# Kernel tuning notes

Measured on AMD Instinct MI355X. Metric: run time of the kernel, lower is better.

Reference implementation:

```python
import jax, jax.numpy as jnp
import numpy as np

NUM_LAYERS = 3
NODE_DIM = 32
TIME_DIM = 32
N_HEAD = 4
N_NODES = 1_000_000
BATCH = 256
MODEL_DIM = NODE_DIM + TIME_DIM  # 64
HEAD_DIM = MODEL_DIM // N_HEAD   # 16


def setup_inputs() -> dict:
    key = jax.random.key(0)
    ks = jax.random.split(key, 20)
    L, D, F = NUM_LAYERS, MODEL_DIM, NODE_DIM
    s = 0.1
    return {
        "src_idx": jax.random.randint(ks[0], (BATCH,), 0, N_NODES),
        "target_idx": jax.random.randint(ks[1], (BATCH,), 0, N_NODES),
        "cut_time": jax.random.uniform(ks[2], (BATCH,), dtype=jnp.float32) * 10000.0,
        "num_neighbors": 20,
        # learned params
        "emb": jax.random.uniform(ks[3], (N_NODES, F), minval=-1.0, maxval=1.0, dtype=jnp.float32),
        "time_freq": (1.0 / 10.0 ** jnp.linspace(0.0, 9.0, TIME_DIM)).astype(jnp.float32),
        "time_phase": jnp.zeros((TIME_DIM,), jnp.float32),
        "Wq": jax.random.normal(ks[4], (L, D, D), jnp.float32) * s,
        "Wk": jax.random.normal(ks[5], (L, D, D), jnp.float32) * s,
        "Wv": jax.random.normal(ks[6], (L, D, D), jnp.float32) * s,
        "Wo": jax.random.normal(ks[7], (L, D, D), jnp.float32) * s,
        "mw1": jax.random.normal(ks[8], (L, D + F, F), jnp.float32) * s,
        "mb1": jnp.zeros((L, F), jnp.float32),
        "mw2": jax.random.normal(ks[9], (L, F, F), jnp.float32) * s,
        "mb2": jnp.zeros((L, F), jnp.float32),
        "aff_w1": jax.random.normal(ks[10], (2 * F, F), jnp.float32) * s,
        "aff_b1": jnp.zeros((F,), jnp.float32),
        "aff_w2": jax.random.normal(ks[11], (F, 1), jnp.float32) * s,
        "aff_b2": jnp.zeros((1,), jnp.float32),
    }


def _time_encode(ts, freq, phase):
    # ts: [...]; output [..., TIME_DIM] harmonic encoding (TGAT TimeEncode)
    return jnp.cos(ts[..., None] * freq + phase)


def _sample_neighbors(nodes, times, num_neighbors):
    # Deterministic stand-in for ngh_finder.get_temporal_neighbor (CPU sampler).
    j = jnp.arange(num_neighbors)
    ngh = (nodes[:, None] * 101 + (j + 1) * 7919) % N_NODES        # [n, K] int
    frac = (j + 1).astype(times.dtype) / (num_neighbors + 1)
    ngh_t = times[:, None] * frac                                  # earlier timestamps
    return ngh, ngh_t


def _attn_layer(l, src_feat, src_t_emb, ngh_feat, ngh_t_emb, mask, p):
    # TGAT-style AttnModel: MHA over [feat||time_emb], then MergeLayer(attn_out, src_feat)
    n, K = ngh_feat.shape[0], ngh_feat.shape[1]
    q_in = jnp.concatenate([src_feat, src_t_emb], axis=-1)            # [n, D]
    k_in = jnp.concatenate([ngh_feat, ngh_t_emb], axis=-1)           # [n, K, D]
    q = (q_in @ p["Wq"][l]).reshape(n, N_HEAD, HEAD_DIM)
    k = (k_in @ p["Wk"][l]).reshape(n, K, N_HEAD, HEAD_DIM)
    v = (k_in @ p["Wv"][l]).reshape(n, K, N_HEAD, HEAD_DIM)
    scores = jnp.einsum("nhd,nkhd->nhk", q, k) / jnp.sqrt(jnp.float32(HEAD_DIM))
    scores = jnp.where(mask[:, None, :], -1e9, scores)
    attn = jax.nn.softmax(scores, axis=-1)
    out = jnp.einsum("nhk,nkhd->nhd", attn, v).reshape(n, MODEL_DIM) @ p["Wo"][l]
    h = jax.nn.relu(jnp.concatenate([out, src_feat], axis=-1) @ p["mw1"][l] + p["mb1"][l])
    return h @ p["mw2"][l] + p["mb2"][l]                              # [n, F]


def _tem_conv(nodes, times, layer, num_neighbors, p):
    feat = p["emb"][nodes]                                            # gather [n, F]
    if layer == 0:
        return feat
    src_conv = _tem_conv(nodes, times, layer - 1, num_neighbors, p)   # [n, F]
    ngh, ngh_t = _sample_neighbors(nodes, times, num_neighbors)       # [n, K]
    delta = times[:, None] - ngh_t                                    # [n, K]
    n = nodes.shape[0]
    ngh_conv = _tem_conv(ngh.reshape(-1), ngh_t.reshape(-1), layer - 1,
                         num_neighbors, p).reshape(n, num_neighbors, NODE_DIM)
    src_t_emb = _time_encode(jnp.zeros_like(times), p["time_freq"], p["time_phase"])  # [n, T]
    ngh_t_emb = _time_encode(delta, p["time_freq"], p["time_phase"])  # [n, K, T]
    mask = ngh == 0
    return _attn_layer(layer - 1, src_conv, src_t_emb, ngh_conv, ngh_t_emb, mask, p)


def reference(src_idx, target_idx, cut_time, num_neighbors, emb, time_freq, time_phase,
              Wq, Wk, Wv, Wo, mw1, mb1, mw2, mb2, aff_w1, aff_b1, aff_w2, aff_b2):
    p = dict(emb=emb, time_freq=time_freq, time_phase=time_phase, Wq=Wq, Wk=Wk, Wv=Wv,
             Wo=Wo, mw1=mw1, mb1=mb1, mw2=mw2, mb2=mb2)
    src_embed = _tem_conv(src_idx, cut_time, NUM_LAYERS, num_neighbors, p)
    tgt_embed = _tem_conv(target_idx, cut_time, NUM_LAYERS, num_neighbors, p)
    h = jax.nn.relu(jnp.concatenate([src_embed, tgt_embed], axis=-1) @ aff_w1 + aff_b1)
    return (h @ aff_w2 + aff_b2).squeeze(-1)                          # [B]
```

## Files before the change

kernel.cpp:

```cpp
#include <hip/hip_runtime.h>
#include <math.h>

#define K 20
#define KP1 21
#define F 32
#define NNODES 1000000

#define NP1 112896
#define NP2 5376
#define NP3 256

#define WBLK 16640
#define OFF_H1 49920
#define OFF_H2 (OFF_H1 + 2 * NP1 * F)
#define OFF_H3 (OFF_H2 + 2 * NP2 * F)

#define LDS_WAVE 16640
#define WV_STRIDE 1648
#define SMEM_FLOATS (LDS_WAVE + 12 * WV_STRIDE)

__device__ __forceinline__ int nhash(int node, int j) {
    return (node * 101 + (j + 1) * 7919) % NNODES;
}

__global__ __launch_bounds__(256) void transform_weights(
    const float* __restrict__ Wq, const float* __restrict__ Wk,
    const float* __restrict__ Wv, const float* __restrict__ Wo,
    const float* __restrict__ mw1, const float* __restrict__ mw2,
    const float* __restrict__ phase, float* __restrict__ ws)
{
    const int l = blockIdx.x, tid = threadIdx.x;
    const float* wq = Wq + l * 4096; const float* wk = Wk + l * 4096;
    const float* wv = Wv + l * 4096; const float* wo = Wo + l * 4096;
    const float* m1 = mw1 + l * 3072; const float* m2 = mw2 + l * 1024;
    float* out = ws + l * WBLK;
    for (int i = tid; i < 8192; i += 256) {
        const int a = i >> 8, e = (i >> 2) & 63, h = i & 3;
        float s = 0.f;
        for (int t = 0; t < 16; ++t) s += wq[a * 64 + h * 16 + t] * wk[e * 64 + h * 16 + t];
        out[i] = s;
    }
    for (int i = tid; i < 256; i += 256) {
        const int e = i >> 2, h = i & 3;
        float s = 0.f;
        for (int a = 0; a < 32; ++a) {
            float acc = 0.f;
            for (int t = 0; t < 16; ++t) acc += wq[(32 + a) * 64 + h * 16 + t] * wk[e * 64 + h * 16 + t];
            s += cosf(phase[a]) * acc;
        }
        out[8192 + i] = s;
    }
    for (int i = tid; i < 4096; i += 256) {
        const int e4 = i >> 8, d = (i >> 2) & 63, c = i & 3;
        out[8448 + i] = wv[(4 * e4 + c) * 64 + d];
    }
    for (int i = tid; i < 3072; i += 256) {
        const int k4 = i >> 7, f = (i >> 2) & 31, c = i & 3;
        const int k = 4 * k4 + c;
        float v;
        if (k < 64) { v = 0.f; for (int g2 = 0; g2 < 64; ++g2) v += wo[k * 64 + g2] * m1[g2 * 32 + f]; }
        else v = m1[k * 32 + f];
        out[12544 + i] = v;
    }
    for (int i = tid; i < 1024; i += 256) {
        const int e4 = i >> 7, d = (i >> 2) & 31, c = i & 3;
        out[15616 + i] = m2[(4 * e4 + c) * 32 + d];
    }
}

template<int LEVEL>
__global__ __launch_bounds__(768) void attn_kernel(
    const int* __restrict__ src_idx, const int* __restrict__ tgt_idx,
    const float* __restrict__ cut_time, const float* __restrict__ emb,
    const float* __restrict__ freq, const float* __restrict__ phase,
    const float* __restrict__ ws_w,
    const float* __restrict__ mb1_, const float* __restrict__ mb2_,
    const float* __restrict__ h_in, float* __restrict__ h_out)
{
    constexpr int NPAIRS = (LEVEL == 1) ? NP1 : (LEVEL == 2 ? NP2 : NP3);
    constexpr int PREVN  = (LEVEL == 2) ? NP1 : NP2;
    constexpr int l = LEVEL - 1;

    extern __shared__ float smem[];

    const int tid  = threadIdx.x;
    const int w    = tid >> 6;
    const int lane = tid & 63;
    const int h    = lane >> 4;
    const int c3   = lane & 7;
    const int rep  = (lane >> 3) & 1;
    const int td   = lane & 31;
    const int half = lane >> 5;

    {
        const float* wsrc = ws_w + l * WBLK;
        for (int i4 = tid; i4 < WBLK / 4; i4 += 768)
            *(float4*)&smem[i4 * 4] = *(const float4*)&wsrc[i4 * 4];
    }
    __syncthreads();

    float* sM   = smem;
    float* sC   = smem + 8192;
    float* sWv4 = smem + 8448;
    float* sP4  = smem + 12544;
    float* sm4  = smem + 15616;
    float* kin  = smem + LDS_WAVE + w * WV_STRIDE;
    float* qfb  = kin + 1280;
    float* qzb  = kin + 1312;
    float* obb  = kin + 1584;

    const float fr = freq[td], ph = phase[td];
    const float b1v = mb1_[l * 32 + td], b2v = mb2_[l * 32 + td];

    const int gstride = gridDim.x * 12;
    float4 pf0, pf1, pf2; int na; float ta;

    auto PRE = [&](int i) {
        const int side = (i >= NPAIRS) ? 1 : 0;
        const int p = i - side * NPAIRS;
        int b, s2 = 0, r = 0;
        if (LEVEL == 3)      { b = p; }
        else if (LEVEL == 2) { b = p / KP1; s2 = p % KP1; }
        else                 { int qq = p / KP1; r = p % KP1; b = qq / KP1; s2 = qq % KP1; }
        const int root = side ? tgt_idx[b] : src_idx[b];
        const float ct = cut_time[b];
        if (LEVEL == 3) { na = root; ta = ct; }
        else if (LEVEL == 2) {
            na = s2 ? nhash(root, s2 - 1) : root;
            ta = s2 ? ct * ((float)s2 / 21.0f) : ct;
        } else {
            const int   n2 = s2 ? nhash(root, s2 - 1) : root;
            const float t2 = s2 ? ct * ((float)s2 / 21.0f) : ct;
            na = r ? nhash(n2, r - 1) : n2;
            ta = r ? t2 * ((float)r / 21.0f) : t2;
        }
        if (LEVEL == 1) {
            { const int row = lane >> 3, c4 = lane & 7;
              const int node = row ? nhash(na, row - 1) : na;
              pf0 = *(const float4*)&emb[(size_t)node * F + c4 * 4]; }
            { const int idx4 = 64 + lane, row = idx4 >> 3, c4 = idx4 & 7;
              const int node = nhash(na, row - 1);
              pf1 = *(const float4*)&emb[(size_t)node * F + c4 * 4]; }
            { const int idx4 = 128 + lane;
              if (idx4 < 168) {
                  const int row = idx4 >> 3, c4 = idx4 & 7;
                  const int node = nhash(na, row - 1);
                  pf2 = *(const float4*)&emb[(size_t)node * F + c4 * 4]; } }
        } else {
            const float* base = h_in + ((size_t)side * PREVN + (size_t)p * KP1) * F;
            pf0 = *(const float4*)&base[lane * 4];
            pf1 = *(const float4*)&base[(64 + lane) * 4];
            if (128 + lane < 168) pf2 = *(const float4*)&base[(128 + lane) * 4];
        }
    };

    int g = blockIdx.x * 12 + w;
    if (g < 2 * NPAIRS) PRE(g);

    for (; g < 2 * NPAIRS; g += gstride) {
        const int curside = (g >= NPAIRS) ? 1 : 0;
        const int curp = g - curside * NPAIRS;
        const int   cna = na;
        const float cta = ta;

        { const int row = lane >> 3, c4 = lane & 7;
          if (row == 0) *(float4*)&qfb[c4 * 4] = pf0;
          else          *(float4*)&kin[(row - 1) * 64 + c4 * 4] = pf0; }
        { const int idx4 = 64 + lane, row = idx4 >> 3, c4 = idx4 & 7;
          *(float4*)&kin[(row - 1) * 64 + c4 * 4] = pf1; }
        { const int idx4 = 128 + lane;
          if (idx4 < 168) { const int row = idx4 >> 3, c4 = idx4 & 7;
            *(float4*)&kin[(row - 1) * 64 + c4 * 4] = pf2; } }

        #pragma unroll
        for (int it = 0; it < 10; ++it) {
            const int j = it * 2 + half;
            const float ngh_t = cta * ((float)(j + 1) / 21.0f);
            const float delta = cta - ngh_t;
            kin[j * 64 + 32 + td] = cosf(delta * fr + ph);
        }
        unsigned mbits = 0;
        { int m = (cna * 101 + 7919) % NNODES;
          #pragma unroll
          for (int j = 0; j < K; ++j) {
              if (m == 0) mbits |= (1u << j);
              m += 7919; if (m >= NNODES) m -= NNODES;
          } }

        if (g + gstride < 2 * NPAIRS) PRE(g + gstride);

        float4 acc = *(const float4*)&sC[lane * 4];
        #pragma unroll
        for (int a4 = 0; a4 < 8; ++a4) {
            const float4 f4 = *(float4*)&qfb[a4 * 4];
            const float4 m0 = *(const float4*)&sM[(a4 * 4 + 0) * 256 + lane * 4];
            const float4 m1v = *(const float4*)&sM[(a4 * 4 + 1) * 256 + lane * 4];
            const float4 m2v = *(const float4*)&sM[(a4 * 4 + 2) * 256 + lane * 4];
            const float4 m3 = *(const float4*)&sM[(a4 * 4 + 3) * 256 + lane * 4];
            acc.x += f4.x * m0.x + f4.y * m1v.x + f4.z * m2v.x + f4.w * m3.x;
            acc.y += f4.x * m0.y + f4.y * m1v.y + f4.z * m2v.y + f4.w * m3.y;
            acc.z += f4.x * m0.z + f4.y * m1v.z + f4.z * m2v.z + f4.w * m3.z;
            acc.w += f4.x * m0.w + f4.y * m1v.w + f4.z * m2v.w + f4.w * m3.w;
        }
        qzb[0 * 68 + lane] = acc.x; qzb[1 * 68 + lane] = acc.y;
        qzb[2 * 68 + lane] = acc.z; qzb[3 * 68 + lane] = acc.w;

        const int ofsA = c3 * 8 + rep * 4;
        const int ofsB = c3 * 8 + 4 - rep * 4;
        const float4 qkA = *(float4*)&qzb[h * 68 + ofsA];
        const float4 qkB = *(float4*)&qzb[h * 68 + ofsB];
        const int j0 = rep * 10;
        float sc[10];
        #pragma unroll
        for (int t = 0; t < 10; ++t) {
            const float4 kA = *(float4*)&kin[(j0 + t) * 64 + ofsA];
            const float4 kB = *(float4*)&kin[(j0 + t) * 64 + ofsB];
            sc[t] = qkA.x * kA.x + qkA.y * kA.y + qkA.z * kA.z + qkA.w * kA.w
                  + qkB.x * kB.x + qkB.y * kB.y + qkB.z * kB.z + qkB.w * kB.w;
        }
        #pragma unroll
        for (int off = 1; off < 8; off <<= 1) {
            #pragma unroll
            for (int t = 0; t < 10; ++t) sc[t] += __shfl_xor(sc[t], off, 8);
        }
        #pragma unroll
        for (int t = 0; t < 10; ++t) {
            float s = sc[t] * 0.25f;
            if ((mbits >> (j0 + t)) & 1) s = -1e9f;
            sc[t] = s;
        }
        float mx = sc[0];
        #pragma unroll
        for (int t = 1; t < 10; ++t) mx = fmaxf(mx, sc[t]);
        mx = fmaxf(mx, __shfl_xor(mx, 8, 16));
        float sum = 0.f;
        #pragma unroll
        for (int t = 0; t < 10; ++t) { sc[t] = __expf(sc[t] - mx); sum += sc[t]; }
        sum += __shfl_xor(sum, 8, 16);
        const float inv = 1.0f / sum;
        float4 zA = {0, 0, 0, 0}, zB = {0, 0, 0, 0};
        #pragma unroll
        for (int t = 0; t < 10; ++t) {
            const float4 kA = *(float4*)&kin[(j0 + t) * 64 + ofsA];
            const float4 kB = *(float4*)&kin[(j0 + t) * 64 + ofsB];
            zA.x += sc[t] * kA.x; zA.y += sc[t] * kA.y; zA.z += sc[t] * kA.z; zA.w += sc[t] * kA.w;
            zB.x += sc[t] * kB.x; zB.y += sc[t] * kB.y; zB.z += sc[t] * kB.z; zB.w += sc[t] * kB.w;
        }
        float4 fA, fB;
        fA.x = zA.x + __shfl_xor(zB.x, 8, 16); fA.y = zA.y + __shfl_xor(zB.y, 8, 16);
        fA.z = zA.z + __shfl_xor(zB.z, 8, 16); fA.w = zA.w + __shfl_xor(zB.w, 8, 16);
        fB.x = zB.x + __shfl_xor(zA.x, 8, 16); fB.y = zB.y + __shfl_xor(zA.y, 8, 16);
        fB.z = zB.z + __shfl_xor(zA.z, 8, 16); fB.w = zB.w + __shfl_xor(zA.w, 8, 16);
        fA.x *= inv; fA.y *= inv; fA.z *= inv; fA.w *= inv;
        fB.x *= inv; fB.y *= inv; fB.z *= inv; fB.w *= inv;
        if (rep == 0) {
            *(float4*)&qzb[h * 68 + ofsA] = fA;
            *(float4*)&qzb[h * 68 + ofsB] = fB;
        }

        float od = 0.f;
        #pragma unroll
        for (int e4 = 0; e4 < 16; ++e4) {
            const float4 z  = *(float4*)&qzb[h * 68 + e4 * 4];
            const float4 wv = *(float4*)&sWv4[e4 * 256 + lane * 4];
            od += z.x * wv.x + z.y * wv.y + z.z * wv.z + z.w * wv.w;
        }
        obb[lane] = od;

        float hv = 0.f;
        #pragma unroll
        for (int e4 = 0; e4 < 12; ++e4) {
            float4 x;
            if (half == 0) x = *(float4*)&obb[e4 * 4];
            else x = (e4 < 4) ? *(float4*)&obb[48 + e4 * 4]
                              : *(float4*)&qfb[(e4 - 4) * 4];
            const float4 w4 = *(float4*)&sP4[(half * 12 + e4) * 128 + td * 4];
            hv += x.x * w4.x + x.y * w4.y + x.z * w4.z + x.w * w4.w;
        }
        hv += __shfl_xor(hv, 32);
        hv = fmaxf(hv + b1v, 0.0f);
        if (lane < 32) obb[td] = hv;

        float y = 0.f;
        #pragma unroll
        for (int e4 = 0; e4 < 4; ++e4) {
            const float4 x  = *(float4*)&obb[half * 16 + e4 * 4];
            const float4 w4 = *(float4*)&sm4[(half * 4 + e4) * 128 + td * 4];
            y += x.x * w4.x + x.y * w4.y + x.z * w4.z + x.w * w4.w;
        }
        y += __shfl_xor(y, 32);
        if (lane < 32)
            h_out[((size_t)curside * NPAIRS + curp) * F + td] = y + b2v;
    }
}

__global__ __launch_bounds__(256) void final_kernel(
    const float* __restrict__ h3,
    const float* __restrict__ aw1, const float* __restrict__ ab1,
    const float* __restrict__ aw2, const float* __restrict__ ab2,
    float* __restrict__ out)
{
    const int bidx = threadIdx.x;
    float x[64];
    #pragma unroll
    for (int e = 0; e < 32; ++e) {
        x[e]      = h3[(size_t)bidx * 32 + e];
        x[32 + e] = h3[((size_t)NP3 + bidx) * 32 + e];
    }
    float acc = ab2[0];
    for (int f = 0; f < 32; ++f) {
        float hv = ab1[f];
        #pragma unroll
        for (int e = 0; e < 64; ++e) hv += x[e] * aw1[e * 32 + f];
        acc += fmaxf(hv, 0.0f) * aw2[f];
    }
    out[bidx] = acc;
}

extern "C" void kernel_launch(void* const* d_in, const int* in_sizes, int n_in,
                              void* d_out, int out_size, void* d_ws, size_t ws_size,
                              hipStream_t stream)
{
    const int*   src_idx = (const int*)d_in[0];
    const int*   tgt_idx = (const int*)d_in[1];
    const float* cut     = (const float*)d_in[2];
    const float* emb   = (const float*)d_in[4];
    const float* freq  = (const float*)d_in[5];
    const float* phase = (const float*)d_in[6];
    const float* Wq    = (const float*)d_in[7];
    const float* Wk    = (const float*)d_in[8];
    const float* Wv    = (const float*)d_in[9];
    const float* Wo    = (const float*)d_in[10];
    const float* mw1   = (const float*)d_in[11];
    const float* mb1   = (const float*)d_in[12];
    const float* mw2   = (const float*)d_in[13];
    const float* mb2   = (const float*)d_in[14];
    const float* aw1   = (const float*)d_in[15];
    const float* ab1   = (const float*)d_in[16];
    const float* aw2   = (const float*)d_in[17];
    const float* ab2   = (const float*)d_in[18];

    float* ws = (float*)d_ws;
    float* h1 = ws + OFF_H1;
    float* h2 = ws + OFF_H2;
    float* h3 = ws + OFF_H3;

    const size_t smem_bytes = SMEM_FLOATS * sizeof(float);
    hipFuncSetAttribute((const void*)attn_kernel<1>, hipFuncAttributeMaxDynamicSharedMemorySize, (int)smem_bytes);
    hipFuncSetAttribute((const void*)attn_kernel<2>, hipFuncAttributeMaxDynamicSharedMemorySize, (int)smem_bytes);
    hipFuncSetAttribute((const void*)attn_kernel<3>, hipFuncAttributeMaxDynamicSharedMemorySize, (int)smem_bytes);

    transform_weights<<<dim3(3), dim3(256), 0, stream>>>(Wq, Wk, Wv, Wo, mw1, mw2, phase, ws);
    attn_kernel<1><<<dim3(256), dim3(768), smem_bytes, stream>>>(
        src_idx, tgt_idx, cut, emb, freq, phase, ws, mb1, mb2, (const float*)nullptr, h1);
    attn_kernel<2><<<dim3(256), dim3(768), smem_bytes, stream>>>(
        src_idx, tgt_idx, cut, emb, freq, phase, ws, mb1, mb2, h1, h2);
    attn_kernel<3><<<dim3(43), dim3(768), smem_bytes, stream>>>(
        src_idx, tgt_idx, cut, emb, freq, phase, ws, mb1, mb2, h2, h3);
    final_kernel<<<dim3(1), dim3(256), 0, stream>>>(h3, aw1, ab1, aw2, ab2, (float*)d_out);
}
```

Baseline: 721.0 us.

## Process two node pairs per wavefront to reuse weight loads, drop P4 from LDS

Each wavefront now handles two (side,pair) items per iteration, so every LDS weight read (sM, sWv4, sm4) feeds two dot products. The P4 MLP weights are read from global memory instead of LDS, which frees space for double per-wave buffers. Blocks shrink from 768 to 512 threads with launch_bounds(512,2) to target two blocks per CU. The cost is higher register pressure from the doubled prefetch state and accumulators, plus global/L1 traffic for P4.

```diff
diff --git a/kernel.cpp b/kernel.cpp
--- a/kernel.cpp
+++ b/kernel.cpp
@@ -15,9 +15,10 @@
 #define OFF_H2 (OFF_H1 + 2 * NP1 * F)
 #define OFF_H3 (OFF_H2 + 2 * NP2 * F)
 
-#define LDS_WAVE 16640
-#define WV_STRIDE 1648
-#define SMEM_FLOATS (LDS_WAVE + 12 * WV_STRIDE)
+#define LDS_M4   12544
+#define LDS_WAVE 13568
+#define WV_STRIDE 3296
+#define SMEM_FLOATS (LDS_WAVE + 8 * WV_STRIDE)
 
 __device__ __forceinline__ int nhash(int node, int j) {
     return (node * 101 + (j + 1) * 7919) % NNODES;
@@ -69,7 +70,7 @@
 }
 
 template<int LEVEL>
-__global__ __launch_bounds__(768) void attn_kernel(
+__global__ __launch_bounds__(512, 2) void attn_kernel(
     const int* __restrict__ src_idx, const int* __restrict__ tgt_idx,
     const float* __restrict__ cut_time, const float* __restrict__ emb,
     const float* __restrict__ freq, const float* __restrict__ phase,
@@ -80,6 +81,7 @@
     constexpr int NPAIRS = (LEVEL == 1) ? NP1 : (LEVEL == 2 ? NP2 : NP3);
     constexpr int PREVN  = (LEVEL == 2) ? NP1 : NP2;
     constexpr int l = LEVEL - 1;
+    constexpr int NBATCH = NPAIRS;
 
     extern __shared__ float smem[];
 
@@ -94,203 +96,258 @@
 
     {
         const float* wsrc = ws_w + l * WBLK;
-        for (int i4 = tid; i4 < WBLK / 4; i4 += 768)
+        for (int i4 = tid; i4 < 3136; i4 += 512)
             *(float4*)&smem[i4 * 4] = *(const float4*)&wsrc[i4 * 4];
+        for (int i4 = tid; i4 < 256; i4 += 512)
+            *(float4*)&smem[LDS_M4 + i4 * 4] = *(const float4*)&wsrc[15616 + i4 * 4];
     }
     __syncthreads();
 
     float* sM   = smem;
     float* sC   = smem + 8192;
     float* sWv4 = smem + 8448;
-    float* sP4  = smem + 12544;
-    float* sm4  = smem + 15616;
-    float* kin  = smem + LDS_WAVE + w * WV_STRIDE;
-    float* qfb  = kin + 1280;
-    float* qzb  = kin + 1312;
-    float* obb  = kin + 1584;
+    float* sm4  = smem + LDS_M4;
+    float* wb   = smem + LDS_WAVE + w * WV_STRIDE;
+    float* kin0 = wb;
+    float* kin1 = wb + 1280;
+    float* qf0  = wb + 2560;
+    float* qf1  = wb + 2592;
+    float* qz0  = wb + 2624;
+    float* qz1  = wb + 2896;
+    float* ob0  = wb + 3168;
+    float* ob1  = wb + 3232;
+
+    const float* P4g = ws_w + l * WBLK + 12544;
 
     const float fr = freq[td], ph = phase[td];
     const float b1v = mb1_[l * 32 + td], b2v = mb2_[l * 32 + td];
 
-    const int gstride = gridDim.x * 12;
-    float4 pf0, pf1, pf2; int na; float ta;
-
-    auto PRE = [&](int i) {
-        const int side = (i >= NPAIRS) ? 1 : 0;
-        const int p = i - side * NPAIRS;
-        int b, s2 = 0, r = 0;
-        if (LEVEL == 3)      { b = p; }
-        else if (LEVEL == 2) { b = p / KP1; s2 = p % KP1; }
-        else                 { int qq = p / KP1; r = p % KP1; b = qq / KP1; s2 = qq % KP1; }
-        const int root = side ? tgt_idx[b] : src_idx[b];
-        const float ct = cut_time[b];
-        if (LEVEL == 3) { na = root; ta = ct; }
-        else if (LEVEL == 2) {
-            na = s2 ? nhash(root, s2 - 1) : root;
-            ta = s2 ? ct * ((float)s2 / 21.0f) : ct;
-        } else {
-            const int   n2 = s2 ? nhash(root, s2 - 1) : root;
-            const float t2 = s2 ? ct * ((float)s2 / 21.0f) : ct;
-            na = r ? nhash(n2, r - 1) : n2;
-            ta = r ? t2 * ((float)r / 21.0f) : t2;
-        }
-        if (LEVEL == 1) {
+    const int gstride = gridDim.x * 8;
+    float4 pf[2][3]; int na[2]; float ta[2];
+
+    auto PRE = [&](int bb) {
+        #pragma unroll
+        for (int q = 0; q < 2; ++q) {
+            const int i    = bb * 2 + q;
+            const int side = (i >= NPAIRS) ? 1 : 0;
+            const int p    = i - side * NPAIRS;
+            int b, s2 = 0, r = 0;
+            if (LEVEL == 3)      { b = p; }
+            else if (LEVEL == 2) { b = p / KP1; s2 = p % KP1; }
+            else                 { int qq = p / KP1; r = p % KP1; b = qq / KP1; s2 = qq % KP1; }
+            const int root = side ? tgt_idx[b] : src_idx[b];
+            const float ct = cut_time[b];
+            int nodeA; float tA;
+            if (LEVEL == 3) { nodeA = root; tA = ct; }
+            else if (LEVEL == 2) {
+                nodeA = s2 ? nhash(root, s2 - 1) : root;
+                tA    = s2 ? ct * ((float)s2 / 21.0f) : ct;
+            } else {
+                const int   n2 = s2 ? nhash(root, s2 - 1) : root;
+                const float t2 = s2 ? ct * ((float)s2 / 21.0f) : ct;
+                nodeA = r ? nhash(n2, r - 1) : n2;
+                tA    = r ? t2 * ((float)r / 21.0f) : t2;
+            }
+            na[q] = nodeA; ta[q] = tA;
+            if (LEVEL == 1) {
+                { const int row = lane >> 3, c4 = lane & 7;
+                  const int node = row ? nhash(nodeA, row - 1) : nodeA;
+                  pf[q][0] = *(const float4*)&emb[(size_t)node * F + c4 * 4]; }
+                { const int idx4 = 64 + lane, row = idx4 >> 3, c4 = idx4 & 7;
+                  const int node = nhash(nodeA, row - 1);
+                  pf[q][1] = *(const float4*)&emb[(size_t)node * F + c4 * 4]; }
+                { const int idx4 = 128 + lane;
+                  if (idx4 < 168) {
+                      const int row = idx4 >> 3, c4 = idx4 & 7;
+                      const int node = nhash(nodeA, row - 1);
+                      pf[q][2] = *(const float4*)&emb[(size_t)node * F + c4 * 4]; } }
+            } else {
+                const float* base = h_in + ((size_t)side * PREVN + (size_t)p * KP1) * F;
+                pf[q][0] = *(const float4*)&base[lane * 4];
+                pf[q][1] = *(const float4*)&base[(64 + lane) * 4];
+                if (128 + lane < 168) pf[q][2] = *(const float4*)&base[(128 + lane) * 4];
+            }
+        }
+    };
+
+    int g = blockIdx.x * 8 + w;
+    if (g < NBATCH) PRE(g);
+
+    for (; g < NBATCH; g += gstride) {
+        const int gs = g;
+        const int cna0 = na[0], cna1 = na[1];
+        const float cta0 = ta[0], cta1 = ta[1];
+
+        #pragma unroll
+        for (int q = 0; q < 2; ++q) {
+            float* kin = q ? kin1 : kin0;
+            float* qfb = q ? qf1 : qf0;
             { const int row = lane >> 3, c4 = lane & 7;
-              const int node = row ? nhash(na, row - 1) : na;
-              pf0 = *(const float4*)&emb[(size_t)node * F + c4 * 4]; }
+              if (row == 0) *(float4*)&qfb[c4 * 4] = pf[q][0];
+              else          *(float4*)&kin[(row - 1) * 64 + c4 * 4] = pf[q][0]; }
             { const int idx4 = 64 + lane, row = idx4 >> 3, c4 = idx4 & 7;
-              const int node = nhash(na, row - 1);
-              pf1 = *(const float4*)&emb[(size_t)node * F + c4 * 4]; }
+              *(float4*)&kin[(row - 1) * 64 + c4 * 4] = pf[q][1]; }
             { const int idx4 = 128 + lane;
-              if (idx4 < 168) {
-                  const int row = idx4 >> 3, c4 = idx4 & 7;
-                  const int node = nhash(na, row - 1);
-                  pf2 = *(const float4*)&emb[(size_t)node * F + c4 * 4]; } }
-        } else {
-            const float* base = h_in + ((size_t)side * PREVN + (size_t)p * KP1) * F;
-            pf0 = *(const float4*)&base[lane * 4];
-            pf1 = *(const float4*)&base[(64 + lane) * 4];
-            if (128 + lane < 168) pf2 = *(const float4*)&base[(128 + lane) * 4];
-        }
-    };
-
-    int g = blockIdx.x * 12 + w;
-    if (g < 2 * NPAIRS) PRE(g);
-
-    for (; g < 2 * NPAIRS; g += gstride) {
-        const int curside = (g >= NPAIRS) ? 1 : 0;
-        const int curp = g - curside * NPAIRS;
-        const int   cna = na;
-        const float cta = ta;
-
-        { const int row = lane >> 3, c4 = lane & 7;
-          if (row == 0) *(float4*)&qfb[c4 * 4] = pf0;
-          else          *(float4*)&kin[(row - 1) * 64 + c4 * 4] = pf0; }
-        { const int idx4 = 64 + lane, row = idx4 >> 3, c4 = idx4 & 7;
-          *(float4*)&kin[(row - 1) * 64 + c4 * 4] = pf1; }
-        { const int idx4 = 128 + lane;
-          if (idx4 < 168) { const int row = idx4 >> 3, c4 = idx4 & 7;
-            *(float4*)&kin[(row - 1) * 64 + c4 * 4] = pf2; } }
+              if (idx4 < 168) { const int row = idx4 >> 3, c4 = idx4 & 7;
+                *(float4*)&kin[(row - 1) * 64 + c4 * 4] = pf[q][2]; } }
+        }
 
         #pragma unroll
         for (int it = 0; it < 10; ++it) {
             const int j = it * 2 + half;
-            const float ngh_t = cta * ((float)(j + 1) / 21.0f);
-            const float delta = cta - ngh_t;
-            kin[j * 64 + 32 + td] = cosf(delta * fr + ph);
-        }
-        unsigned mbits = 0;
-        { int m = (cna * 101 + 7919) % NNODES;
+            { const float ngh_t = cta0 * ((float)(j + 1) / 21.0f);
+              const float delta = cta0 - ngh_t;
+              kin0[j * 64 + 32 + td] = cosf(delta * fr + ph); }
+            { const float ngh_t = cta1 * ((float)(j + 1) / 21.0f);
+              const float delta = cta1 - ngh_t;
+              kin1[j * 64 + 32 + td] = cosf(delta * fr + ph); }
+        }
+        unsigned mb[2];
+        { int m = (cna0 * 101 + 7919) % NNODES; unsigned bits = 0;
           #pragma unroll
-          for (int j = 0; j < K; ++j) {
-              if (m == 0) mbits |= (1u << j);
-              m += 7919; if (m >= NNODES) m -= NNODES;
-          } }
-
-        if (g + gstride < 2 * NPAIRS) PRE(g + gstride);
-
-        float4 acc = *(const float4*)&sC[lane * 4];
+          for (int j = 0; j < K; ++j) { if (m == 0) bits |= (1u << j); m += 7919; if (m >= NNODES) m -= NNODES; }
+          mb[0] = bits; }
+        { int m = (cna1 * 101 + 7919) % NNODES; unsigned bits = 0;
+          #pragma unroll
+          for (int j = 0; j < K; ++j) { if (m == 0) bits |= (1u << j); m += 7919; if (m >= NNODES) m -= NNODES; }
+          mb[1] = bits; }
+
+        if (g + gstride < NBATCH) PRE(g + gstride);
+
+        float4 acc0 = *(const float4*)&sC[lane * 4];
+        float4 acc1 = acc0;
         #pragma unroll
         for (int a4 = 0; a4 < 8; ++a4) {
-            const float4 f4 = *(float4*)&qfb[a4 * 4];
+            const float4 f0 = *(float4*)&qf0[a4 * 4];
+            const float4 f1 = *(float4*)&qf1[a4 * 4];
             const float4 m0 = *(const float4*)&sM[(a4 * 4 + 0) * 256 + lane * 4];
             const float4 m1v = *(const float4*)&sM[(a4 * 4 + 1) * 256 + lane * 4];
             const float4 m2v = *(const float4*)&sM[(a4 * 4 + 2) * 256 + lane * 4];
             const float4 m3 = *(const float4*)&sM[(a4 * 4 + 3) * 256 + lane * 4];
-            acc.x += f4.x * m0.x + f4.y * m1v.x + f4.z * m2v.x + f4.w * m3.x;
-            acc.y += f4.x * m0.y + f4.y * m1v.y + f4.z * m2v.y + f4.w * m3.y;
-            acc.z += f4.x * m0.z + f4.y * m1v.z + f4.z * m2v.z + f4.w * m3.z;
-            acc.w += f4.x * m0.w + f4.y * m1v.w + f4.z * m2v.w + f4.w * m3.w;
-        }
-        qzb[0 * 68 + lane] = acc.x; qzb[1 * 68 + lane] = acc.y;
-        qzb[2 * 68 + lane] = acc.z; qzb[3 * 68 + lane] = acc.w;
+            acc0.x += f0.x * m0.x + f0.y * m1v.x + f0.z * m2v.x + f0.w * m3.x;
+            acc0.y += f0.x * m0.y + f0.y * m1v.y + f0.z * m2v.y + f0.w * m3.y;
+            acc0.z += f0.x * m0.z + f0.y * m1v.z + f0.z * m2v.z + f0.w * m3.z;
+            acc0.w += f0.x * m0.w + f0.y * m1v.w + f0.z * m2v.w + f0.w * m3.w;
+            acc1.x += f1.x * m0.x + f1.y * m1v.x + f1.z * m2v.x + f1.w * m3.x;
+            acc1.y += f1.x * m0.y + f1.y * m1v.y + f1.z * m2v.y + f1.w * m3.y;
+            acc1.z += f1.x * m0.z + f1.y * m1v.z + f1.z * m2v.z + f1.w * m3.z;
+            acc1.w += f1.x * m0.w + f1.y * m1v.w + f1.z * m2v.w + f1.w * m3.w;
+        }
+        qz0[0 * 68 + lane] = acc0.x; qz0[1 * 68 + lane] = acc0.y;
+        qz0[2 * 68 + lane] = acc0.z; qz0[3 * 68 + lane] = acc0.w;
+        qz1[0 * 68 + lane] = acc1.x; qz1[1 * 68 + lane] = acc1.y;
+        qz1[2 * 68 + lane] = acc1.z; qz1[3 * 68 + lane] = acc1.w;
 
         const int ofsA = c3 * 8 + rep * 4;
         const int ofsB = c3 * 8 + 4 - rep * 4;
-        const float4 qkA = *(float4*)&qzb[h * 68 + ofsA];
-        const float4 qkB = *(float4*)&qzb[h * 68 + ofsB];
         const int j0 = rep * 10;
-        float sc[10];
-        #pragma unroll
-        for (int t = 0; t < 10; ++t) {
-            const float4 kA = *(float4*)&kin[(j0 + t) * 64 + ofsA];
-            const float4 kB = *(float4*)&kin[(j0 + t) * 64 + ofsB];
-            sc[t] = qkA.x * kA.x + qkA.y * kA.y + qkA.z * kA.z + qkA.w * kA.w
-                  + qkB.x * kB.x + qkB.y * kB.y + qkB.z * kB.z + qkB.w * kB.w;
-        }
-        #pragma unroll
-        for (int off = 1; off < 8; off <<= 1) {
-            #pragma unroll
-            for (int t = 0; t < 10; ++t) sc[t] += __shfl_xor(sc[t], off, 8);
-        }
-        #pragma unroll
-        for (int t = 0; t < 10; ++t) {
-            float s = sc[t] * 0.25f;
-            if ((mbits >> (j0 + t)) & 1) s = -1e9f;
-            sc[t] = s;
-        }
-        float mx = sc[0];
-        #pragma unroll
-        for (int t = 1; t < 10; ++t) mx = fmaxf(mx, sc[t]);
-        mx = fmaxf(mx, __shfl_xor(mx, 8, 16));
-        float sum = 0.f;
-        #pragma unroll
-        for (int t = 0; t < 10; ++t) { sc[t] = __expf(sc[t] - mx); sum += sc[t]; }
-        sum += __shfl_xor(sum, 8, 16);
-        const float inv = 1.0f / sum;
-        float4 zA = {0, 0, 0, 0}, zB = {0, 0, 0, 0};
-        #pragma unroll
-        for (int t = 0; t < 10; ++t) {
-            const float4 kA = *(float4*)&kin[(j0 + t) * 64 + ofsA];
-            const float4 kB = *(float4*)&kin[(j0 + t) * 64 + ofsB];
-            zA.x += sc[t] * kA.x; zA.y += sc[t] * kA.y; zA.z += sc[t] * kA.z; zA.w += sc[t] * kA.w;
-            zB.x += sc[t] * kB.x; zB.y += sc[t] * kB.y; zB.z += sc[t] * kB.z; zB.w += sc[t] * kB.w;
-        }
-        float4 fA, fB;
-        fA.x = zA.x + __shfl_xor(zB.x, 8, 16); fA.y = zA.y + __shfl_xor(zB.y, 8, 16);
-        fA.z = zA.z + __shfl_xor(zB.z, 8, 16); fA.w = zA.w + __shfl_xor(zB.w, 8, 16);
-        fB.x = zB.x + __shfl_xor(zA.x, 8, 16); fB.y = zB.y + __shfl_xor(zA.y, 8, 16);
-        fB.z = zB.z + __shfl_xor(zA.z, 8, 16); fB.w = zB.w + __shfl_xor(zA.w, 8, 16);
-        fA.x *= inv; fA.y *= inv; fA.z *= inv; fA.w *= inv;
-        fB.x *= inv; fB.y *= inv; fB.z *= inv; fB.w *= inv;
-        if (rep == 0) {
-            *(float4*)&qzb[h * 68 + ofsA] = fA;
-            *(float4*)&qzb[h * 68 + ofsB] = fB;
-        }
-
-        float od = 0.f;
+        #pragma unroll
+        for (int q = 0; q < 2; ++q) {
+            float* kin = q ? kin1 : kin0;
+            float* qzb = q ? qz1 : qz0;
+            const float4 qkA = *(float4*)&qzb[h * 68 + ofsA];
+            const float4 qkB = *(float4*)&qzb[h * 68 + ofsB];
+            float sc[10];
+            #pragma unroll
+            for (int t = 0; t < 10; ++t) {
+                const float4 kA = *(float4*)&kin[(j0 + t) * 64 + ofsA];
+                const float4 kB = *(float4*)&kin[(j0 + t) * 64 + ofsB];
+                sc[t] = qkA.x * kA.x + qkA.y * kA.y + qkA.z * kA.z + qkA.w * kA.w
+                      + qkB.x * kB.x + qkB.y * kB.y + qkB.z * kB.z + qkB.w * kB.w;
+            }
+            #pragma unroll
+            for (int off = 1; off < 8; off <<= 1) {
+                #pragma unroll
+                for (int t = 0; t < 10; ++t) sc[t] += __shfl_xor(sc[t], off, 8);
+            }
+            #pragma unroll
+            for (int t = 0; t < 10; ++t) {
+                float s = sc[t] * 0.25f;
+                if ((mb[q] >> (j0 + t)) & 1) s = -1e9f;
+                sc[t] = s;
+            }
+            float mx = sc[0];
+            #pragma unroll
+            for (int t = 1; t < 10; ++t) mx = fmaxf(mx, sc[t]);
+            mx = fmaxf(mx, __shfl_xor(mx, 8, 16));
+            float sum = 0.f;
+            #pragma unroll
+            for (int t = 0; t < 10; ++t) { sc[t] = __expf(sc[t] - mx); sum += sc[t]; }
+            sum += __shfl_xor(sum, 8, 16);
+            const float inv = 1.0f / sum;
+            float4 zA = {0, 0, 0, 0}, zB = {0, 0, 0, 0};
+            #pragma unroll
+            for (int t = 0; t < 10; ++t) {
+                const float4 kA = *(float4*)&kin[(j0 + t) * 64 + ofsA];
+                const float4 kB = *(float4*)&kin[(j0 + t) * 64 + ofsB];
+                zA.x += sc[t] * kA.x; zA.y += sc[t] * kA.y; zA.z += sc[t] * kA.z; zA.w += sc[t] * kA.w;
+                zB.x += sc[t] * kB.x; zB.y += sc[t] * kB.y; zB.z += sc[t] * kB.z; zB.w += sc[t] * kB.w;
+            }
+            float4 fA, fB;
+            fA.x = zA.x + __shfl_xor(zB.x, 8, 16); fA.y = zA.y + __shfl_xor(zB.y, 8, 16);
+            fA.z = zA.z + __shfl_xor(zB.z, 8, 16); fA.w = zA.w + __shfl_xor(zB.w, 8, 16);
+            fB.x = zB.x + __shfl_xor(zA.x, 8, 16); fB.y = zB.y + __shfl_xor(zA.y, 8, 16);
+            fB.z = zB.z + __shfl_xor(zA.z, 8, 16); fB.w = zB.w + __shfl_xor(zA.w, 8, 16);
+            fA.x *= inv; fA.y *= inv; fA.z *= inv; fA.w *= inv;
+            fB.x *= inv; fB.y *= inv; fB.z *= inv; fB.w *= inv;
+            if (rep == 0) {
+                *(float4*)&qzb[h * 68 + ofsA] = fA;
+                *(float4*)&qzb[h * 68 + ofsB] = fB;
+            }
+        }
+
+        float od0 = 0.f, od1 = 0.f;
         #pragma unroll
         for (int e4 = 0; e4 < 16; ++e4) {
-            const float4 z  = *(float4*)&qzb[h * 68 + e4 * 4];
             const float4 wv = *(float4*)&sWv4[e4 * 256 + lane * 4];
-            od += z.x * wv.x + z.y * wv.y + z.z * wv.z + z.w * wv.w;
-        }
-        obb[lane] = od;
-
-        float hv = 0.f;
+            const float4 z0 = *(float4*)&qz0[h * 68 + e4 * 4];
+            const float4 z1 = *(float4*)&qz1[h * 68 + e4 * 4];
+            od0 += z0.x * wv.x + z0.y * wv.y + z0.z * wv.z + z0.w * wv.w;
+            od1 += z1.x * wv.x + z1.y * wv.y + z1.z * wv.z + z1.w * wv.w;
+        }
+        ob0[lane] = od0;
+        ob1[lane] = od1;
+
+        float hv0 = 0.f, hv1 = 0.f;
         #pragma unroll
         for (int e4 = 0; e4 < 12; ++e4) {
-            float4 x;
-            if (half == 0) x = *(float4*)&obb[e4 * 4];
-            else x = (e4 < 4) ? *(float4*)&obb[48 + e4 * 4]
-                              : *(float4*)&qfb[(e4 - 4) * 4];
-            const float4 w4 = *(float4*)&sP4[(half * 12 + e4) * 128 + td * 4];
-            hv += x.x * w4.x + x.y * w4.y + x.z * w4.z + x.w * w4.w;
-        }
-        hv += __shfl_xor(hv, 32);
-        hv = fmaxf(hv + b1v, 0.0f);
-        if (lane < 32) obb[td] = hv;
-
-        float y = 0.f;
+            float4 x0, x1;
+            if (half == 0) { x0 = *(float4*)&ob0[e4 * 4]; x1 = *(float4*)&ob1[e4 * 4]; }
+            else {
+                x0 = (e4 < 4) ? *(float4*)&ob0[48 + e4 * 4] : *(float4*)&qf0[(e4 - 4) * 4];
+                x1 = (e4 < 4) ? *(float4*)&ob1[48 + e4 * 4] : *(float4*)&qf1[(e4 - 4) * 4];
+            }
+            const float4 w4 = *(const float4*)&P4g[(half * 12 + e4) * 128 + td * 4];
+            hv0 += x0.x * w4.x + x0.y * w4.y + x0.z * w4.z + x0.w * w4.w;
+            hv1 += x1.x * w4.x + x1.y * w4.y + x1.z * w4.z + x1.w * w4.w;
+        }
+        hv0 += __shfl_xor(hv0, 32);
+        hv1 += __shfl_xor(hv1, 32);
+        hv0 = fmaxf(hv0 + b1v, 0.0f);
+        hv1 = fmaxf(hv1 + b1v, 0.0f);
+        if (lane < 32) { ob0[td] = hv0; ob1[td] = hv1; }
+
+        float y0 = 0.f, y1 = 0.f;
         #pragma unroll
         for (int e4 = 0; e4 < 4; ++e4) {
-            const float4 x  = *(float4*)&obb[half * 16 + e4 * 4];
             const float4 w4 = *(float4*)&sm4[(half * 4 + e4) * 128 + td * 4];
-            y += x.x * w4.x + x.y * w4.y + x.z * w4.z + x.w * w4.w;
-        }
-        y += __shfl_xor(y, 32);
-        if (lane < 32)
-            h_out[((size_t)curside * NPAIRS + curp) * F + td] = y + b2v;
+            const float4 x0 = *(float4*)&ob0[half * 16 + e4 * 4];
+            const float4 x1 = *(float4*)&ob1[half * 16 + e4 * 4];
+            y0 += x0.x * w4.x + x0.y * w4.y + x0.z * w4.z + x0.w * w4.w;
+            y1 += x1.x * w4.x + x1.y * w4.y + x1.z * w4.z + x1.w * w4.w;
+        }
+        y0 += __shfl_xor(y0, 32);
+        y1 += __shfl_xor(y1, 32);
+        if (lane < 32) {
+            #pragma unroll
+            for (int q = 0; q < 2; ++q) {
+                const int i    = gs * 2 + q;
+                const int side = (i >= NPAIRS) ? 1 : 0;
+                const int p    = i - side * NPAIRS;
+                const float y  = (q == 0) ? y0 : y1;
+                h_out[((size_t)side * NPAIRS + p) * F + td] = y + b2v;
+            }
+        }
     }
 }
 
@@ -351,11 +408,11 @@
     hipFuncSetAttribute((const void*)attn_kernel<3>, hipFuncAttributeMaxDynamicSharedMemorySize, (int)smem_bytes);
 
     transform_weights<<<dim3(3), dim3(256), 0, stream>>>(Wq, Wk, Wv, Wo, mw1, mw2, phase, ws);
-    attn_kernel<1><<<dim3(256), dim3(768), smem_bytes, stream>>>(
+    attn_kernel<1><<<dim3(256), dim3(512), smem_bytes, stream>>>(
         src_idx, tgt_idx, cut, emb, freq, phase, ws, mb1, mb2, (const float*)nullptr, h1);
-    attn_kernel<2><<<dim3(256), dim3(768), smem_bytes, stream>>>(
+    attn_kernel<2><<<dim3(256), dim3(512), smem_bytes, stream>>>(
         src_idx, tgt_idx, cut, emb, freq, phase, ws, mb1, mb2, h1, h2);
-    attn_kernel<3><<<dim3(43), dim3(768), smem_bytes, stream>>>(
+    attn_kernel<3><<<dim3(32), dim3(512), smem_bytes, stream>>>(
         src_idx, tgt_idx, cut, emb, freq, phase, ws, mb1, mb2, h2, h3);
     final_kernel<<<dim3(1), dim3(256), 0, stream>>>(h3, aw1, ab1, aw2, ab2, (float*)d_out);
 }
```

New measurement: 797.5 us. 10.6% more time.

## Use single-pass softmax, fast cosine, closed-form mask, and trimmed LDS weights

Applied to the files above, without the earlier changes.

Folds the 1/sqrt(head_dim) scale into the precomputed QK weight matrices. Fuses score computation, masking, exponentiation and value accumulation into one loop with no max subtraction. Replaces cosf with a range-reduced hardware cosine and the 20-step mask loop with a closed-form division. Reads the MLP first-layer weights from global memory instead of LDS, which shrinks the per-block LDS footprint. Dropping the max subtraction assumes scores stay small enough not to overflow exp, and a fully masked row would now divide by zero instead of giving uniform weights.

```diff
diff --git a/kernel.cpp b/kernel.cpp
--- a/kernel.cpp
+++ b/kernel.cpp
@@ -15,12 +15,30 @@
 #define OFF_H2 (OFF_H1 + 2 * NP1 * F)
 #define OFF_H3 (OFF_H2 + 2 * NP2 * F)
 
-#define LDS_WAVE 16640
+#define LDS_M4   12544
+#define LDS_WAVE 13568
 #define WV_STRIDE 1648
 #define SMEM_FLOATS (LDS_WAVE + 12 * WV_STRIDE)
 
 __device__ __forceinline__ int nhash(int node, int j) {
     return (node * 101 + (j + 1) * 7919) % NNODES;
+}
+
+__device__ __forceinline__ float fast_cosf(float x) {
+    const float inv2pi = 0.15915494309189535f;
+    const float k = rintf(x * inv2pi);
+    float r = fmaf(k, -6.28125f, x);
+    r = fmaf(k, -1.9353071795864769e-3f, r);
+    float rev = __builtin_amdgcn_fractf(r * inv2pi);
+    return __builtin_amdgcn_cosf(rev);
+}
+
+__device__ __forceinline__ unsigned mask_bits(int na) {
+    const int m0 = (na * 101) % NNODES;
+    const unsigned d = (unsigned)(NNODES - m0);
+    const unsigned q = d / 7919u;
+    const unsigned rem = d - q * 7919u;
+    return (rem == 0u && (q - 1u) < 20u) ? (1u << (q - 1u)) : 0u;
 }
 
 __global__ __launch_bounds__(256) void transform_weights(
@@ -38,7 +56,7 @@
         const int a = i >> 8, e = (i >> 2) & 63, h = i & 3;
         float s = 0.f;
         for (int t = 0; t < 16; ++t) s += wq[a * 64 + h * 16 + t] * wk[e * 64 + h * 16 + t];
-        out[i] = s;
+        out[i] = s * 0.25f;
     }
     for (int i = tid; i < 256; i += 256) {
         const int e = i >> 2, h = i & 3;
@@ -48,7 +66,7 @@
             for (int t = 0; t < 16; ++t) acc += wq[(32 + a) * 64 + h * 16 + t] * wk[e * 64 + h * 16 + t];
             s += cosf(phase[a]) * acc;
         }
-        out[8192 + i] = s;
+        out[8192 + i] = s * 0.25f;
     }
     for (int i = tid; i < 4096; i += 256) {
         const int e4 = i >> 8, d = (i >> 2) & 63, c = i & 3;
@@ -94,26 +112,39 @@
 
     {
         const float* wsrc = ws_w + l * WBLK;
-        for (int i4 = tid; i4 < WBLK / 4; i4 += 768)
+        for (int i4 = tid; i4 < 3136; i4 += 768)
             *(float4*)&smem[i4 * 4] = *(const float4*)&wsrc[i4 * 4];
+        for (int i4 = tid; i4 < 256; i4 += 768)
+            *(float4*)&smem[LDS_M4 + i4 * 4] = *(const float4*)&wsrc[15616 + i4 * 4];
     }
     __syncthreads();
 
     float* sM   = smem;
     float* sC   = smem + 8192;
     float* sWv4 = smem + 8448;
-    float* sP4  = smem + 12544;
-    float* sm4  = smem + 15616;
-    float* kin  = smem + LDS_WAVE + w * WV_STRIDE;
-    float* qfb  = kin + 1280;
-    float* qzb  = kin + 1312;
-    float* obb  = kin + 1584;
+    float* sm4  = smem + LDS_M4;
+    float* wb   = smem + LDS_WAVE + w * WV_STRIDE;
+    float* kin  = wb;
+    float* qfb  = wb + 1280;
+    float* qzb  = wb + 1312;
+    float* obb  = wb + 1584;
+
+    const float* P4g = ws_w + l * WBLK + 12544;
 
     const float fr = freq[td], ph = phase[td];
     const float b1v = mb1_[l * 32 + td], b2v = mb2_[l * 32 + td];
 
+    const int ofsA = c3 * 8 + rep * 4;
+    const int ofsB = c3 * 8 + 4 - rep * 4;
+    const int j0 = rep * 10;
+
     const int gstride = gridDim.x * 12;
     float4 pf0, pf1, pf2; int na; float ta;
+
+    const int prow  = lane >> 3, pc4 = lane & 7;
+    const int prow1 = (64 + lane) >> 3, pc41 = (64 + lane) & 7;
+    const int idx42 = 128 + lane;
+    const int prow2 = idx42 >> 3, pc42 = idx42 & 7;
 
     auto PRE = [&](int i) {
         const int side = (i >= NPAIRS) ? 1 : 0;
@@ -135,22 +166,18 @@
             ta = r ? t2 * ((float)r / 21.0f) : t2;
         }
         if (LEVEL == 1) {
-            { const int row = lane >> 3, c4 = lane & 7;
-              const int node = row ? nhash(na, row - 1) : na;
-              pf0 = *(const float4*)&emb[(size_t)node * F + c4 * 4]; }
-            { const int idx4 = 64 + lane, row = idx4 >> 3, c4 = idx4 & 7;
-              const int node = nhash(na, row - 1);
-              pf1 = *(const float4*)&emb[(size_t)node * F + c4 * 4]; }
-            { const int idx4 = 128 + lane;
-              if (idx4 < 168) {
-                  const int row = idx4 >> 3, c4 = idx4 & 7;
-                  const int node = nhash(na, row - 1);
-                  pf2 = *(const float4*)&emb[(size_t)node * F + c4 * 4]; } }
+            { const int node = prow ? nhash(na, prow - 1) : na;
+              pf0 = *(const float4*)&emb[(size_t)node * F + pc4 * 4]; }
+            { const int node = nhash(na, prow1 - 1);
+              pf1 = *(const float4*)&emb[(size_t)node * F + pc41 * 4]; }
+            if (idx42 < 168) {
+              const int node = nhash(na, prow2 - 1);
+              pf2 = *(const float4*)&emb[(size_t)node * F + pc42 * 4]; }
         } else {
             const float* base = h_in + ((size_t)side * PREVN + (size_t)p * KP1) * F;
             pf0 = *(const float4*)&base[lane * 4];
             pf1 = *(const float4*)&base[(64 + lane) * 4];
-            if (128 + lane < 168) pf2 = *(const float4*)&base[(128 + lane) * 4];
+            if (idx42 < 168) pf2 = *(const float4*)&base[idx42 * 4];
         }
     };
 
@@ -158,34 +185,23 @@
     if (g < 2 * NPAIRS) PRE(g);
 
     for (; g < 2 * NPAIRS; g += gstride) {
-        const int curside = (g >= NPAIRS) ? 1 : 0;
-        const int curp = g - curside * NPAIRS;
-        const int   cna = na;
+        const int gs = g;
+        const int cna = na;
         const float cta = ta;
 
-        { const int row = lane >> 3, c4 = lane & 7;
-          if (row == 0) *(float4*)&qfb[c4 * 4] = pf0;
-          else          *(float4*)&kin[(row - 1) * 64 + c4 * 4] = pf0; }
-        { const int idx4 = 64 + lane, row = idx4 >> 3, c4 = idx4 & 7;
-          *(float4*)&kin[(row - 1) * 64 + c4 * 4] = pf1; }
-        { const int idx4 = 128 + lane;
-          if (idx4 < 168) { const int row = idx4 >> 3, c4 = idx4 & 7;
-            *(float4*)&kin[(row - 1) * 64 + c4 * 4] = pf2; } }
+        { if (prow == 0) *(float4*)&qfb[pc4 * 4] = pf0;
+          else           *(float4*)&kin[(prow - 1) * 64 + pc4 * 4] = pf0; }
+        *(float4*)&kin[(prow1 - 1) * 64 + pc41 * 4] = pf1;
+        if (idx42 < 168) *(float4*)&kin[(prow2 - 1) * 64 + pc42 * 4] = pf2;
 
         #pragma unroll
         for (int it = 0; it < 10; ++it) {
             const int j = it * 2 + half;
             const float ngh_t = cta * ((float)(j + 1) / 21.0f);
             const float delta = cta - ngh_t;
-            kin[j * 64 + 32 + td] = cosf(delta * fr + ph);
-        }
-        unsigned mbits = 0;
-        { int m = (cna * 101 + 7919) % NNODES;
-          #pragma unroll
-          for (int j = 0; j < K; ++j) {
-              if (m == 0) mbits |= (1u << j);
-              m += 7919; if (m >= NNODES) m -= NNODES;
-          } }
+            kin[j * 64 + 32 + td] = fast_cosf(delta * fr + ph);
+        }
+        const unsigned mbits = mask_bits(cna);
 
         if (g + gstride < 2 * NPAIRS) PRE(g + gstride);
 
@@ -205,57 +221,39 @@
         qzb[0 * 68 + lane] = acc.x; qzb[1 * 68 + lane] = acc.y;
         qzb[2 * 68 + lane] = acc.z; qzb[3 * 68 + lane] = acc.w;
 
-        const int ofsA = c3 * 8 + rep * 4;
-        const int ofsB = c3 * 8 + 4 - rep * 4;
-        const float4 qkA = *(float4*)&qzb[h * 68 + ofsA];
-        const float4 qkB = *(float4*)&qzb[h * 68 + ofsB];
-        const int j0 = rep * 10;
-        float sc[10];
-        #pragma unroll
-        for (int t = 0; t < 10; ++t) {
-            const float4 kA = *(float4*)&kin[(j0 + t) * 64 + ofsA];
-            const float4 kB = *(float4*)&kin[(j0 + t) * 64 + ofsB];
-            sc[t] = qkA.x * kA.x + qkA.y * kA.y + qkA.z * kA.z + qkA.w * kA.w
-                  + qkB.x * kB.x + qkB.y * kB.y + qkB.z * kB.z + qkB.w * kB.w;
-        }
-        #pragma unroll
-        for (int off = 1; off < 8; off <<= 1) {
+        {
+            const float4 qkA = *(float4*)&qzb[h * 68 + ofsA];
+            const float4 qkB = *(float4*)&qzb[h * 68 + ofsB];
+            float4 zA = {0, 0, 0, 0}, zB = {0, 0, 0, 0};
+            float sum = 0.f;
             #pragma unroll
-            for (int t = 0; t < 10; ++t) sc[t] += __shfl_xor(sc[t], off, 8);
-        }
-        #pragma unroll
-        for (int t = 0; t < 10; ++t) {
-            float s = sc[t] * 0.25f;
-            if ((mbits >> (j0 + t)) & 1) s = -1e9f;
-            sc[t] = s;
-        }
-        float mx = sc[0];
-        #pragma unroll
-        for (int t = 1; t < 10; ++t) mx = fmaxf(mx, sc[t]);
-        mx = fmaxf(mx, __shfl_xor(mx, 8, 16));
-        float sum = 0.f;
-        #pragma unroll
-        for (int t = 0; t < 10; ++t) { sc[t] = __expf(sc[t] - mx); sum += sc[t]; }
-        sum += __shfl_xor(sum, 8, 16);
-        const float inv = 1.0f / sum;
-        float4 zA = {0, 0, 0, 0}, zB = {0, 0, 0, 0};
-        #pragma unroll
-        for (int t = 0; t < 10; ++t) {
-            const float4 kA = *(float4*)&kin[(j0 + t) * 64 + ofsA];
-            const float4 kB = *(float4*)&kin[(j0 + t) * 64 + ofsB];
-            zA.x += sc[t] * kA.x; zA.y += sc[t] * kA.y; zA.z += sc[t] * kA.z; zA.w += sc[t] * kA.w;
-            zB.x += sc[t] * kB.x; zB.y += sc[t] * kB.y; zB.z += sc[t] * kB.z; zB.w += sc[t] * kB.w;
-        }
-        float4 fA, fB;
-        fA.x = zA.x + __shfl_xor(zB.x, 8, 16); fA.y = zA.y + __shfl_xor(zB.y, 8, 16);
-        fA.z = zA.z + __shfl_xor(zB.z, 8, 16); fA.w = zA.w + __shfl_xor(zB.w, 8, 16);
-        fB.x = zB.x + __shfl_xor(zA.x, 8, 16); fB.y = zB.y + __shfl_xor(zA.y, 8, 16);
-        fB.z = zB.z + __shfl_xor(zA.z, 8, 16); fB.w = zB.w + __shfl_xor(zA.w, 8, 16);
-        fA.x *= inv; fA.y *= inv; fA.z *= inv; fA.w *= inv;
-        fB.x *= inv; fB.y *= inv; fB.z *= inv; fB.w *= inv;
-        if (rep == 0) {
-            *(float4*)&qzb[h * 68 + ofsA] = fA;
-            *(float4*)&qzb[h * 68 + ofsB] = fB;
+            for (int t = 0; t < 10; ++t) {
+                const float4 kA = *(float4*)&kin[(j0 + t) * 64 + ofsA];
+                const float4 kB = *(float4*)&kin[(j0 + t) * 64 + ofsB];
+                float s = qkA.x * kA.x + qkA.y * kA.y + qkA.z * kA.z + qkA.w * kA.w
+                        + qkB.x * kB.x + qkB.y * kB.y + qkB.z * kB.z + qkB.w * kB.w;
+                s += __shfl_xor(s, 1, 16);
+                s += __shfl_xor(s, 2, 16);
+                s += __shfl_xor(s, 4, 16);
+                if ((mbits >> (j0 + t)) & 1) s = -1e9f;
+                const float p = __expf(s);
+                sum += p;
+                zA.x += p * kA.x; zA.y += p * kA.y; zA.z += p * kA.z; zA.w += p * kA.w;
+                zB.x += p * kB.x; zB.y += p * kB.y; zB.z += p * kB.z; zB.w += p * kB.w;
+            }
+            sum += __shfl_xor(sum, 8, 16);
+            const float inv = 1.0f / sum;
+            float4 fA, fB;
+            fA.x = zA.x + __shfl_xor(zB.x, 8, 16); fA.y = zA.y + __shfl_xor(zB.y, 8, 16);
+            fA.z = zA.z + __shfl_xor(zB.z, 8, 16); fA.w = zA.w + __shfl_xor(zB.w, 8, 16);
+            fB.x = zB.x + __shfl_xor(zA.x, 8, 16); fB.y = zB.y + __shfl_xor(zA.y, 8, 16);
+            fB.z = zB.z + __shfl_xor(zA.z, 8, 16); fB.w = zB.w + __shfl_xor(zA.w, 8, 16);
+            fA.x *= inv; fA.y *= inv; fA.z *= inv; fA.w *= inv;
+            fB.x *= inv; fB.y *= inv; fB.z *= inv; fB.w *= inv;
+            if (rep == 0) {
+                *(float4*)&qzb[h * 68 + ofsA] = fA;
+                *(float4*)&qzb[h * 68 + ofsB] = fB;
+            }
         }
 
         float od = 0.f;
@@ -274,7 +272,7 @@
             if (half == 0) x = *(float4*)&obb[e4 * 4];
             else x = (e4 < 4) ? *(float4*)&obb[48 + e4 * 4]
                               : *(float4*)&qfb[(e4 - 4) * 4];
-            const float4 w4 = *(float4*)&sP4[(half * 12 + e4) * 128 + td * 4];
+            const float4 w4 = *(const float4*)&P4g[(half * 12 + e4) * 128 + td * 4];
             hv += x.x * w4.x + x.y * w4.y + x.z * w4.z + x.w * w4.w;
         }
         hv += __shfl_xor(hv, 32);
@@ -289,8 +287,11 @@
             y += x.x * w4.x + x.y * w4.y + x.z * w4.z + x.w * w4.w;
         }
         y += __shfl_xor(y, 32);
-        if (lane < 32)
-            h_out[((size_t)curside * NPAIRS + curp) * F + td] = y + b2v;
+        if (lane < 32) {
+            const int side = (gs >= NPAIRS) ? 1 : 0;
+            const int p = gs - side * NPAIRS;
+            h_out[((size_t)side * NPAIRS + p) * F + td] = y + b2v;
+        }
     }
 }
 
```

Result: slower. 1.655 ms (+129.6%).
